# Performance work log

Hardware: AMD Instinct MI355X
Metric: run time of the kernel (lower is better)

## Reference

```python
import jax, jax.numpy as jnp
import numpy as np

N_EMBD = 768
N_HEAD = 12
HEAD_DIM = N_EMBD // N_HEAD


def setup_inputs() -> dict:
    key = jax.random.key(0)
    ks = jax.random.split(key, 5)
    B, S = 4, 2048
    x = jax.random.normal(ks[0], (B, S, N_EMBD), dtype=jnp.float32)
    scale = 0.02
    w_attn = jax.random.normal(ks[1], (N_EMBD, 3 * N_EMBD), dtype=jnp.float32) * scale
    b_attn = jnp.zeros((3 * N_EMBD,), dtype=jnp.float32)
    w_proj = jax.random.normal(ks[2], (N_EMBD, N_EMBD), dtype=jnp.float32) * scale
    b_proj = jnp.zeros((N_EMBD,), dtype=jnp.float32)
    return {"x": x, "w_attn": w_attn, "b_attn": b_attn, "w_proj": w_proj, "b_proj": b_proj}


def reference(x, w_attn, b_attn, w_proj, b_proj):
    B, S, E = x.shape
    qkv = x @ w_attn + b_attn  # [B,S,3E]
    q, k, v = jnp.split(qkv, 3, axis=2)
    # [B,H,S,D]
    q = q.reshape(B, S, N_HEAD, HEAD_DIM).transpose(0, 2, 1, 3)
    k = k.reshape(B, S, N_HEAD, HEAD_DIM).transpose(0, 2, 1, 3)
    v = v.reshape(B, S, N_HEAD, HEAD_DIM).transpose(0, 2, 1, 3)
    scores = jnp.einsum('bhqd,bhkd->bhqk', q, k) / jnp.sqrt(jnp.float32(HEAD_DIM))
    causal = jnp.tril(jnp.ones((S, S), dtype=bool))
    scores = jnp.where(causal[None, None], scores, jnp.float32(-jnp.inf))
    weights = jax.nn.softmax(scores, axis=-1)
    out = jnp.einsum('bhqk,bhkd->bhqd', weights, v)
    out = out.transpose(0, 2, 1, 3).reshape(B, S, E)
    return out @ w_proj + b_proj
```

## Files before the change

### kernel.cpp

```cpp
#include <hip/hip_runtime.h>
#include <hip/hip_bf16.h>

typedef __attribute__((ext_vector_type(8))) __bf16 bf16x8;
typedef __attribute__((ext_vector_type(4))) __bf16 bf16x4;
typedef __attribute__((ext_vector_type(4))) float f32x4;

#define E_ 768
#define HEADS 12
#define HD 64
#define S_ 2048
#define B_ 4

__device__ inline unsigned short f2bf(float f) {
    union { float f; unsigned int u; } x{f};
    unsigned int r = x.u + 0x7FFFu + ((x.u >> 16) & 1u);
    return (unsigned short)(r >> 16);
}

__device__ inline float fexp2(float x) { return __builtin_amdgcn_exp2f(x); }

__global__ void cvt_kernel(const float* __restrict__ in, unsigned short* __restrict__ out, int n4) {
    int i = blockIdx.x * blockDim.x + threadIdx.x;
    if (i < n4) {
        float4 v = reinterpret_cast<const float4*>(in)[i];
        ushort4 o;
        o.x = f2bf(v.x); o.y = f2bf(v.y); o.z = f2bf(v.z); o.w = f2bf(v.w);
        reinterpret_cast<ushort4*>(out)[i] = o;
    }
}

__global__ void transpose_cvt(const float* __restrict__ w, unsigned short* __restrict__ wT,
                              int K, int N) {
    __shared__ float tile[32][33];
    int n0 = blockIdx.x * 32, k0 = blockIdx.y * 32;
    int tx = threadIdx.x, ty = threadIdx.y;
    tile[ty][tx] = w[(size_t)(k0 + ty) * N + n0 + tx];
    __syncthreads();
    wT[(size_t)(n0 + ty) * K + k0 + tx] = f2bf(tile[tx][ty]);
}

template<int MODE>
__global__ __launch_bounds__(256) void gemm16(
    const unsigned short* __restrict__ A, const unsigned short* __restrict__ Bt,
    const float* __restrict__ bias,
    unsigned short* __restrict__ Qo, unsigned short* __restrict__ Ko,
    unsigned short* __restrict__ Vt, float* __restrict__ Of,
    int M, int N, int K)
{
    constexpr int BN = (MODE == 0) ? 128 : 64;
    constexpr int NJ = BN / 32;
    __shared__ unsigned short Sh[128 * 128];
    unsigned short* Ash = Sh;
    unsigned short* Bsh = Sh + 128 * 64;

    const int nbx = N / BN;
    const int nwg = (M >> 7) * nbx;
    const int cpx = nwg >> 3;
    const int orig = blockIdx.x;
    const int wgid = (orig & 7) * cpx + (orig >> 3);
    const int row0 = (wgid / nbx) * 128;
    const int col0 = (wgid % nbx) * BN;

    const int t = threadIdx.x;
    const int w = t >> 6, lane = t & 63;
    const int lr = lane & 15, lc = lane >> 4;
    const int wrow = (w >> 1) * 64;
    const int wcol = (w & 1) * (BN / 2);

    const int srow = lane >> 3;
    const int sslot = lane & 7;

    f32x4 acc[4][NJ] = {};

    for (int k0 = 0; k0 < K; k0 += 64) {
#pragma unroll
        for (int j = 0; j < 4; j++) {
            const int rbase = j * 32 + w * 8;
            const unsigned short* ga = A + (size_t)(row0 + rbase + srow) * K + k0 + sslot * 8;
            __builtin_amdgcn_global_load_lds(
                (const __attribute__((address_space(1))) void*)ga,
                (__attribute__((address_space(3))) void*)&Ash[rbase * 64], 16, 0, 0);
        }
#pragma unroll
        for (int j = 0; j < NJ; j++) {
            const int rbase = j * 32 + w * 8;
            const unsigned short* gb = Bt + (size_t)(col0 + rbase + srow) * K + k0 + sslot * 8;
            __builtin_amdgcn_global_load_lds(
                (const __attribute__((address_space(1))) void*)gb,
                (__attribute__((address_space(3))) void*)&Bsh[rbase * 64], 16, 0, 0);
        }
        __syncthreads();

#pragma unroll
        for (int ks = 0; ks < 2; ks++) {
            bf16x8 a[4], b[NJ];
#pragma unroll
            for (int i = 0; i < 4; i++)
                a[i] = *reinterpret_cast<const bf16x8*>(&Ash[(wrow + i * 16 + lr) * 64 + ks * 32 + lc * 8]);
#pragma unroll
            for (int j2 = 0; j2 < NJ; j2++)
                b[j2] = *reinterpret_cast<const bf16x8*>(&Bsh[(wcol + j2 * 16 + lr) * 64 + ks * 32 + lc * 8]);
#pragma unroll
            for (int i = 0; i < 4; i++)
#pragma unroll
                for (int j2 = 0; j2 < NJ; j2++)
                    acc[i][j2] = __builtin_amdgcn_mfma_f32_16x16x32_bf16(a[i], b[j2], acc[i][j2], 0, 0, 0);
        }
        __syncthreads();
    }

    if constexpr (MODE == 0) {
        const int bb = row0 >> 11;
        const int s0 = row0 & (S_ - 1);
        if (col0 >= 2 * E_) {
#pragma unroll
            for (int i = 0; i < 4; i++)
#pragma unroll
                for (int j = 0; j < 4; j++) {
                    const int c = wcol + j * 16 + lr;
                    const float bv = bias[col0 + c];
#pragma unroll
                    for (int r = 0; r < 4; r++) {
                        const int row = wrow + i * 16 + lc * 4 + r;
                        Sh[c * 128 + (row ^ ((c & 15) << 3))] = f2bf(acc[i][j][r] + bv);
                    }
                }
            __syncthreads();
            const int nnb = col0 - 2 * E_;
#pragma unroll
            for (int pass = 0; pass < 8; pass++) {
                const int c = pass * 16 + (t >> 4);
                const int sL = (t & 15) * 8;
                bf16x8 vv = *reinterpret_cast<const bf16x8*>(&Sh[c * 128 + (sL ^ ((c & 15) << 3))]);
                const int h = (nnb + c) >> 6, d = c & 63;
                const size_t bh = (size_t)(bb * HEADS + h);
                *reinterpret_cast<bf16x8*>(&Vt[(bh * HD + d) * S_ + s0 + sL]) = vv;
            }
            return;
        }
        const int which = col0 / E_;
        const float qsc = (which == 0) ? 0.18033688f : 1.0f;
        unsigned short* dst = (which == 0) ? Qo : Ko;
        const int hbase = (col0 - which * E_) >> 6;
#pragma unroll
        for (int i = 0; i < 4; i++)
#pragma unroll
            for (int j = 0; j < 4; j++) {
                const int c = wcol + j * 16 + lr;
                const float bv = bias[col0 + c];
#pragma unroll
                for (int r = 0; r < 4; r++) {
                    const int row = wrow + i * 16 + lc * 4 + r;
                    Sh[row * 128 + (c ^ ((row & 15) << 3))] = f2bf((acc[i][j][r] + bv) * qsc);
                }
            }
        __syncthreads();
#pragma unroll
        for (int pass = 0; pass < 8; pass++) {
            const int row = pass * 16 + (t >> 4);
            const int c2 = (t & 15) * 8;
            bf16x8 vv = *reinterpret_cast<const bf16x8*>(&Sh[row * 128 + (c2 ^ ((row & 15) << 3))]);
            const int h = hbase + (c2 >> 6), d = c2 & 63;
            const size_t bh = (size_t)(bb * HEADS + h);
            *reinterpret_cast<bf16x8*>(&dst[(bh * S_ + s0 + row) * HD + d]) = vv;
        }
    } else {
#pragma unroll
        for (int i = 0; i < 4; i++)
#pragma unroll
            for (int j = 0; j < NJ; j++) {
                int col = col0 + wcol + j * 16 + lr;
                float bv = bias[col];
#pragma unroll
                for (int r = 0; r < 4; r++) {
                    int row = row0 + wrow + i * 16 + lc * 4 + r;
                    Of[(size_t)row * N + col] = acc[i][j][r] + bv;
                }
            }
    }
}

__global__ __launch_bounds__(256) void attn_kernel(
    const unsigned short* __restrict__ Q, const unsigned short* __restrict__ Kd,
    const unsigned short* __restrict__ Vt, unsigned short* __restrict__ O)
{
    __shared__ unsigned short Ksh[128 * 64];
    __shared__ unsigned short Vsh[64 * 128];

    const int t = threadIdx.x;
    const int w = t >> 6, lane = t & 63;
    const int lr = lane & 15, lc = lane >> 4;
    const int g = blockIdx.x;
    const int bp = g / 48;
    const int bh = g - bp * 48;
    const int tTL = bp, tTH = 31 - bp;
    const int qLrow0 = tTL * 64 + w * 16;
    const int qHrow0 = tTH * 64 + w * 16;
    const int nL = (tTL + 2) >> 1;

    const unsigned short* Qb = Q + (size_t)bh * S_ * HD;
    const unsigned short* Kb = Kd + (size_t)bh * S_ * HD;
    const unsigned short* Vb = Vt + (size_t)bh * HD * S_;

    const int srK = t >> 3, ssK = t & 7;
    const int kws = ((ssK ^ (srK & 7)) << 3);
    const int srV = t >> 4, ssV = t & 15;
    const int vs1 = (ssV >> 2) * 4 + (ssV & 1) * 2;
    const int voff = ((ssV >> 1) & 1) * 4;
    const int vws1 = ((vs1 ^ srV) << 3) + voff;
    const int vws2 = (((vs1 + 1) ^ srV) << 3) + voff;
    const int r7 = lr & 7;

    const unsigned short* KbS = Kb + (size_t)srK * HD + ssK * 8;
    const unsigned short* VbS = Vb + (size_t)srV * S_ + ssV * 8;

    bf16x8 aqL[2], aqH[2];
#pragma unroll
    for (int dc = 0; dc < 2; dc++) {
        aqL[dc] = *reinterpret_cast<const bf16x8*>(Qb + (size_t)(qLrow0 + lr) * HD + dc * 32 + lc * 8);
        aqH[dc] = *reinterpret_cast<const bf16x8*>(Qb + (size_t)(qHrow0 + lr) * HD + dc * 32 + lc * 8);
    }

    f32x4 o[4] = {};
    float m = -INFINITY, l = 0.f;

    int bb = bh / HEADS, hh = bh - bb * HEADS;

    bf16x8 kreg[4], vreg[4];
#pragma unroll
    for (int i = 0; i < 4; i++) {
        kreg[i] = *reinterpret_cast<const bf16x8*>(KbS + i * 32 * HD);
        vreg[i] = *reinterpret_cast<const bf16x8*>(VbS + i * 16 * S_);
    }

    bf16x8 aq0 = aqL[0], aq1 = aqL[1];
    int qrow = qLrow0 + lr;

    for (int it = 0; it < 17; ++it) {
        __syncthreads();
#pragma unroll
        for (int i = 0; i < 4; i++) {
            *reinterpret_cast<bf16x8*>(&Ksh[(srK + i * 32) * 64 + kws]) = kreg[i];
            union { bf16x8 v; bf16x4 h[2]; } u;
            u.v = vreg[i];
            const int vrow = (srV + i * 16) * 128;
            *reinterpret_cast<bf16x4*>(&Vsh[vrow + vws1]) = u.h[0];
            *reinterpret_cast<bf16x4*>(&Vsh[vrow + vws2]) = u.h[1];
        }
        __syncthreads();

        if (it + 1 < 17) {
            const int nkv0 = (it + 1 < nL) ? (it + 1) * 128 : (it + 1 - nL) * 128;
#pragma unroll
            for (int i = 0; i < 4; i++) {
                kreg[i] = *reinterpret_cast<const bf16x8*>(KbS + (size_t)nkv0 * HD + i * 32 * HD);
                vreg[i] = *reinterpret_cast<const bf16x8*>(VbS + nkv0 + i * 16 * S_);
            }
        }

        if (it == nL) {
            float lq[4];
#pragma unroll
            for (int r = 0; r < 4; r++) lq[r] = __shfl(l, lc * 4 + r);
#pragma unroll
            for (int r = 0; r < 4; r++) {
                float inv = 1.f / lq[r];
                int qr = qLrow0 + lc * 4 + r;
#pragma unroll
                for (int dt = 0; dt < 4; dt++)
                    O[((size_t)(bb * S_ + qr)) * E_ + hh * HD + dt * 16 + lr] = f2bf(o[dt][r] * inv);
            }
            m = -INFINITY; l = 0.f;
#pragma unroll
            for (int dt = 0; dt < 4; dt++)
#pragma unroll
                for (int r = 0; r < 4; r++) o[dt][r] = 0.f;
            aq0 = aqH[0]; aq1 = aqH[1];
            qrow = qHrow0 + lr;
        }

        const int kv0 = (it < nL) ? it * 128 : (it - nL) * 128;
        const bool needMask = (it == nL - 1) || (it == 16);

        float p[8][4];
#pragma unroll
        for (int kt = 0; kt < 8; kt++) {
            const int row = kt * 16 + lr;
            const bf16x8 bk0 = *reinterpret_cast<const bf16x8*>(&Ksh[row * 64 + ((lc ^ r7) << 3)]);
            const bf16x8 bk1 = *reinterpret_cast<const bf16x8*>(&Ksh[row * 64 + (((4 + lc) ^ r7) << 3)]);
            f32x4 s = {};
            s = __builtin_amdgcn_mfma_f32_16x16x32_bf16(bk0, aq0, s, 0, 0, 0);
            s = __builtin_amdgcn_mfma_f32_16x16x32_bf16(bk1, aq1, s, 0, 0, 0);
#pragma unroll
            for (int r = 0; r < 4; r++) p[kt][r] = s[r];
        }
        if (needMask) {
#pragma unroll
            for (int kt = 0; kt < 8; kt++) {
                const int kbase = kv0 + kt * 16 + lc * 4;
#pragma unroll
                for (int r = 0; r < 4; r++)
                    if (kbase + r > qrow) p[kt][r] = -1e30f;
            }
        }

        float rm = -1e30f;
#pragma unroll
        for (int kt = 0; kt < 8; kt++)
#pragma unroll
            for (int r = 0; r < 4; r++) rm = fmaxf(rm, p[kt][r]);
        rm = fmaxf(rm, __shfl_xor(rm, 16));
        rm = fmaxf(rm, __shfl_xor(rm, 32));

        const bool grow = !__all(rm <= m);
        float mn = m, sc;
        if (grow) {
            mn = fmaxf(m, rm);
            sc = fexp2(m - mn);
        }

        float rs = 0.f;
#pragma unroll
        for (int kt = 0; kt < 8; kt++)
#pragma unroll
            for (int r = 0; r < 4; r++) {
                float e = fexp2(p[kt][r] - mn);
                p[kt][r] = e; rs += e;
            }
        rs += __shfl_xor(rs, 16);
        rs += __shfl_xor(rs, 32);

        if (grow) {
            l = l * sc + rs;
            m = mn;
            float scq[4];
#pragma unroll
            for (int r = 0; r < 4; r++) scq[r] = __shfl(sc, lc * 4 + r);
#pragma unroll
            for (int dt = 0; dt < 4; dt++)
#pragma unroll
                for (int r = 0; r < 4; r++) o[dt][r] *= scq[r];
        } else {
            l += rs;
        }

        bf16x8 ap[4];
#pragma unroll
        for (int kc = 0; kc < 4; kc++) {
            union { bf16x8 v; __bf16 b[8]; } u;
            u.b[0] = (__bf16)p[2 * kc][0];     u.b[1] = (__bf16)p[2 * kc][1];
            u.b[2] = (__bf16)p[2 * kc][2];     u.b[3] = (__bf16)p[2 * kc][3];
            u.b[4] = (__bf16)p[2 * kc + 1][0]; u.b[5] = (__bf16)p[2 * kc + 1][1];
            u.b[6] = (__bf16)p[2 * kc + 1][2]; u.b[7] = (__bf16)p[2 * kc + 1][3];
            ap[kc] = u.v;
        }

#pragma unroll
        for (int dt = 0; dt < 4; dt++) {
            const int row = dt * 16 + lr;
#pragma unroll
            for (int kc = 0; kc < 4; kc++) {
                const bf16x8 bv = *reinterpret_cast<const bf16x8*>(
                    &Vsh[row * 128 + (((kc * 4 + lc) ^ lr) << 3)]);
                o[dt] = __builtin_amdgcn_mfma_f32_16x16x32_bf16(ap[kc], bv, o[dt], 0, 0, 0);
            }
        }
    }

    {
        float lq[4];
#pragma unroll
        for (int r = 0; r < 4; r++) lq[r] = __shfl(l, lc * 4 + r);
#pragma unroll
        for (int r = 0; r < 4; r++) {
            float inv = 1.f / lq[r];
            int qr = qHrow0 + lc * 4 + r;
#pragma unroll
            for (int dt = 0; dt < 4; dt++)
                O[((size_t)(bb * S_ + qr)) * E_ + hh * HD + dt * 16 + lr] = f2bf(o[dt][r] * inv);
        }
    }
}

extern "C" void kernel_launch(void* const* d_in, const int* in_sizes, int n_in,
                              void* d_out, int out_size, void* d_ws, size_t ws_size,
                              hipStream_t stream) {
    const float* x      = (const float*)d_in[0];
    const float* w_attn = (const float*)d_in[1];
    const float* b_attn = (const float*)d_in[2];
    const float* w_proj = (const float*)d_in[3];
    const float* b_proj = (const float*)d_in[4];
    float* out = (float*)d_out;

    char* ws = (char*)d_ws;
    const size_t M = (size_t)B_ * S_;
    unsigned short* xb  = (unsigned short*)(ws);
    unsigned short* waT = (unsigned short*)(ws + 12582912);
    unsigned short* wpT = (unsigned short*)(ws + 16121856);
    unsigned short* Qb  = (unsigned short*)(ws + 17301504);
    unsigned short* Kb  = (unsigned short*)(ws + 29884416);
    unsigned short* Vt  = (unsigned short*)(ws + 42467328);
    unsigned short* AO  = (unsigned short*)(ws + 55050240);

    int n4 = (int)(M * E_ / 4);
    cvt_kernel<<<(n4 + 255) / 256, 256, 0, stream>>>(x, xb, n4);
    transpose_cvt<<<dim3(3 * E_ / 32, E_ / 32), dim3(32, 32), 0, stream>>>(w_attn, waT, E_, 3 * E_);
    transpose_cvt<<<dim3(E_ / 32, E_ / 32), dim3(32, 32), 0, stream>>>(w_proj, wpT, E_, E_);

    gemm16<0><<<1152, 256, 0, stream>>>(
        xb, waT, b_attn, Qb, Kb, Vt, nullptr, (int)M, 3 * E_, E_);

    attn_kernel<<<768, 256, 0, stream>>>(Qb, Kb, Vt, AO);

    gemm16<1><<<768, 256, 0, stream>>>(
        AO, wpT, b_proj, nullptr, nullptr, nullptr, out, (int)M, E_, E_);
}
```

Baseline: 159.0 us.

## Software-pipeline attention loop: overlap QK^T of next tile with softmax/PV of previous

Restructures the attention main loop into epochs in which the QK^T MFMAs for tile e run alongside the softmax and PV MFMAs for tile e-1. V shared memory is double-buffered, and K/V global prefetches are staggered so K is loaded two tiles ahead and V one tile ahead. The aim is to hide softmax latency and LDS stores behind matrix work and cut idle time between dependent phases. In exchange it uses more registers (two score arrays) and more LDS, which could lower occupancy.

```diff
diff --git a/kernel.cpp b/kernel.cpp
--- a/kernel.cpp
+++ b/kernel.cpp
@@ -185,7 +185,7 @@
     const unsigned short* __restrict__ Vt, unsigned short* __restrict__ O)
 {
     __shared__ unsigned short Ksh[128 * 64];
-    __shared__ unsigned short Vsh[64 * 128];
+    __shared__ unsigned short Vsh[2][64 * 128];
 
     const int t = threadIdx.x;
     const int w = t >> 6, lane = t & 63;
@@ -193,9 +193,9 @@
     const int g = blockIdx.x;
     const int bp = g / 48;
     const int bh = g - bp * 48;
-    const int tTL = bp, tTH = 31 - bp;
+    const int tTL = bp;
     const int qLrow0 = tTL * 64 + w * 16;
-    const int qHrow0 = tTH * 64 + w * 16;
+    const int qHrow0 = (31 - bp) * 64 + w * 16;
     const int nL = (tTL + 2) >> 1;
 
     const unsigned short* Qb = Q + (size_t)bh * S_ * HD;
@@ -223,148 +223,174 @@
 
     f32x4 o[4] = {};
     float m = -INFINITY, l = 0.f;
-
-    int bb = bh / HEADS, hh = bh - bb * HEADS;
+    const int bb = bh / HEADS, hh = bh - bb * HEADS;
+
+    auto KV0 = [&](int tIdx) { return (tIdx < nL ? tIdx : tIdx - nL) * 128; };
 
     bf16x8 kreg[4], vreg[4];
 #pragma unroll
-    for (int i = 0; i < 4; i++) {
+    for (int i = 0; i < 4; i++)
         kreg[i] = *reinterpret_cast<const bf16x8*>(KbS + i * 32 * HD);
-        vreg[i] = *reinterpret_cast<const bf16x8*>(VbS + i * 16 * S_);
-    }
-
-    bf16x8 aq0 = aqL[0], aq1 = aqL[1];
-    int qrow = qLrow0 + lr;
-
-    for (int it = 0; it < 17; ++it) {
-        __syncthreads();
+#pragma unroll
+    for (int i = 0; i < 4; i++)
+        *reinterpret_cast<bf16x8*>(&Ksh[(srK + i * 32) * 64 + kws]) = kreg[i];
+    {
+        const int k1 = KV0(1), v0 = 0;
 #pragma unroll
         for (int i = 0; i < 4; i++) {
-            *reinterpret_cast<bf16x8*>(&Ksh[(srK + i * 32) * 64 + kws]) = kreg[i];
-            union { bf16x8 v; bf16x4 h[2]; } u;
-            u.v = vreg[i];
-            const int vrow = (srV + i * 16) * 128;
-            *reinterpret_cast<bf16x4*>(&Vsh[vrow + vws1]) = u.h[0];
-            *reinterpret_cast<bf16x4*>(&Vsh[vrow + vws2]) = u.h[1];
-        }
-        __syncthreads();
-
-        if (it + 1 < 17) {
-            const int nkv0 = (it + 1 < nL) ? (it + 1) * 128 : (it + 1 - nL) * 128;
+            kreg[i] = *reinterpret_cast<const bf16x8*>(KbS + (size_t)k1 * HD + i * 32 * HD);
+            vreg[i] = *reinterpret_cast<const bf16x8*>(VbS + v0 + i * 16 * S_);
+        }
+    }
+    __syncthreads();
+
+    float pA[8][4], pB[8][4];
+
+    auto epoch = [&](int e, float (&pcur)[8][4], float (&pprev)[8][4]) {
+        if (e < 17) {
+            const bf16x8 aq0 = (e < nL) ? aqL[0] : aqH[0];
+            const bf16x8 aq1 = (e < nL) ? aqL[1] : aqH[1];
+#pragma unroll
+            for (int kt = 0; kt < 8; kt++) {
+                const int row = kt * 16 + lr;
+                const bf16x8 bk0 = *reinterpret_cast<const bf16x8*>(&Ksh[row * 64 + ((lc ^ r7) << 3)]);
+                const bf16x8 bk1 = *reinterpret_cast<const bf16x8*>(&Ksh[row * 64 + (((4 + lc) ^ r7) << 3)]);
+                f32x4 s = {};
+                s = __builtin_amdgcn_mfma_f32_16x16x32_bf16(bk0, aq0, s, 0, 0, 0);
+                s = __builtin_amdgcn_mfma_f32_16x16x32_bf16(bk1, aq1, s, 0, 0, 0);
+#pragma unroll
+                for (int r = 0; r < 4; r++) pcur[kt][r] = s[r];
+            }
+            __syncthreads();
 #pragma unroll
             for (int i = 0; i < 4; i++) {
-                kreg[i] = *reinterpret_cast<const bf16x8*>(KbS + (size_t)nkv0 * HD + i * 32 * HD);
-                vreg[i] = *reinterpret_cast<const bf16x8*>(VbS + nkv0 + i * 16 * S_);
-            }
-        }
-
-        if (it == nL) {
-            float lq[4];
-#pragma unroll
-            for (int r = 0; r < 4; r++) lq[r] = __shfl(l, lc * 4 + r);
-#pragma unroll
-            for (int r = 0; r < 4; r++) {
-                float inv = 1.f / lq[r];
-                int qr = qLrow0 + lc * 4 + r;
+                if (e <= 15)
+                    *reinterpret_cast<bf16x8*>(&Ksh[(srK + i * 32) * 64 + kws]) = kreg[i];
+                union { bf16x8 v; bf16x4 h[2]; } u;
+                u.v = vreg[i];
+                const int vrow = (srV + i * 16) * 128;
+                *reinterpret_cast<bf16x4*>(&Vsh[e & 1][vrow + vws1]) = u.h[0];
+                *reinterpret_cast<bf16x4*>(&Vsh[e & 1][vrow + vws2]) = u.h[1];
+            }
+            if (e <= 14) {
+                const int kk = KV0(e + 2);
+#pragma unroll
+                for (int i = 0; i < 4; i++)
+                    kreg[i] = *reinterpret_cast<const bf16x8*>(KbS + (size_t)kk * HD + i * 32 * HD);
+            }
+            if (e <= 15) {
+                const int vv = KV0(e + 1);
+#pragma unroll
+                for (int i = 0; i < 4; i++)
+                    vreg[i] = *reinterpret_cast<const bf16x8*>(VbS + vv + i * 16 * S_);
+            }
+        }
+
+        if (e >= 1) {
+            const int tIdx = e - 1;
+            const bool lightT = tIdx < nL;
+            const int qrow_t = (lightT ? qLrow0 : qHrow0) + lr;
+            const int kv0_t = (lightT ? tIdx : tIdx - nL) * 128;
+            if (tIdx == nL - 1 || tIdx == 16) {
+#pragma unroll
+                for (int kt = 0; kt < 8; kt++) {
+                    const int kbase = kv0_t + kt * 16 + lc * 4;
+#pragma unroll
+                    for (int r = 0; r < 4; r++)
+                        if (kbase + r > qrow_t) pprev[kt][r] = -1e30f;
+                }
+            }
+
+            float rm = -1e30f;
+#pragma unroll
+            for (int kt = 0; kt < 8; kt++)
+#pragma unroll
+                for (int r = 0; r < 4; r++) rm = fmaxf(rm, pprev[kt][r]);
+            rm = fmaxf(rm, __shfl_xor(rm, 16));
+            rm = fmaxf(rm, __shfl_xor(rm, 32));
+
+            const bool grow = !__all(rm <= m);
+            float mn = m, sc;
+            if (grow) {
+                mn = fmaxf(m, rm);
+                sc = fexp2(m - mn);
+            }
+
+            float rs = 0.f;
+#pragma unroll
+            for (int kt = 0; kt < 8; kt++)
+#pragma unroll
+                for (int r = 0; r < 4; r++) {
+                    float ee = fexp2(pprev[kt][r] - mn);
+                    pprev[kt][r] = ee; rs += ee;
+                }
+            rs += __shfl_xor(rs, 16);
+            rs += __shfl_xor(rs, 32);
+
+            if (grow) {
+                l = l * sc + rs;
+                m = mn;
+                float scq[4];
+#pragma unroll
+                for (int r = 0; r < 4; r++) scq[r] = __shfl(sc, lc * 4 + r);
 #pragma unroll
                 for (int dt = 0; dt < 4; dt++)
-                    O[((size_t)(bb * S_ + qr)) * E_ + hh * HD + dt * 16 + lr] = f2bf(o[dt][r] * inv);
-            }
-            m = -INFINITY; l = 0.f;
-#pragma unroll
-            for (int dt = 0; dt < 4; dt++)
-#pragma unroll
-                for (int r = 0; r < 4; r++) o[dt][r] = 0.f;
-            aq0 = aqH[0]; aq1 = aqH[1];
-            qrow = qHrow0 + lr;
-        }
-
-        const int kv0 = (it < nL) ? it * 128 : (it - nL) * 128;
-        const bool needMask = (it == nL - 1) || (it == 16);
-
-        float p[8][4];
-#pragma unroll
-        for (int kt = 0; kt < 8; kt++) {
-            const int row = kt * 16 + lr;
-            const bf16x8 bk0 = *reinterpret_cast<const bf16x8*>(&Ksh[row * 64 + ((lc ^ r7) << 3)]);
-            const bf16x8 bk1 = *reinterpret_cast<const bf16x8*>(&Ksh[row * 64 + (((4 + lc) ^ r7) << 3)]);
-            f32x4 s = {};
-            s = __builtin_amdgcn_mfma_f32_16x16x32_bf16(bk0, aq0, s, 0, 0, 0);
-            s = __builtin_amdgcn_mfma_f32_16x16x32_bf16(bk1, aq1, s, 0, 0, 0);
-#pragma unroll
-            for (int r = 0; r < 4; r++) p[kt][r] = s[r];
-        }
-        if (needMask) {
-#pragma unroll
-            for (int kt = 0; kt < 8; kt++) {
-                const int kbase = kv0 + kt * 16 + lc * 4;
-#pragma unroll
-                for (int r = 0; r < 4; r++)
-                    if (kbase + r > qrow) p[kt][r] = -1e30f;
-            }
-        }
-
-        float rm = -1e30f;
-#pragma unroll
-        for (int kt = 0; kt < 8; kt++)
-#pragma unroll
-            for (int r = 0; r < 4; r++) rm = fmaxf(rm, p[kt][r]);
-        rm = fmaxf(rm, __shfl_xor(rm, 16));
-        rm = fmaxf(rm, __shfl_xor(rm, 32));
-
-        const bool grow = !__all(rm <= m);
-        float mn = m, sc;
-        if (grow) {
-            mn = fmaxf(m, rm);
-            sc = fexp2(m - mn);
-        }
-
-        float rs = 0.f;
-#pragma unroll
-        for (int kt = 0; kt < 8; kt++)
-#pragma unroll
-            for (int r = 0; r < 4; r++) {
-                float e = fexp2(p[kt][r] - mn);
-                p[kt][r] = e; rs += e;
-            }
-        rs += __shfl_xor(rs, 16);
-        rs += __shfl_xor(rs, 32);
-
-        if (grow) {
-            l = l * sc + rs;
-            m = mn;
-            float scq[4];
-#pragma unroll
-            for (int r = 0; r < 4; r++) scq[r] = __shfl(sc, lc * 4 + r);
-#pragma unroll
-            for (int dt = 0; dt < 4; dt++)
-#pragma unroll
-                for (int r = 0; r < 4; r++) o[dt][r] *= scq[r];
-        } else {
-            l += rs;
-        }
-
-        bf16x8 ap[4];
-#pragma unroll
-        for (int kc = 0; kc < 4; kc++) {
-            union { bf16x8 v; __bf16 b[8]; } u;
-            u.b[0] = (__bf16)p[2 * kc][0];     u.b[1] = (__bf16)p[2 * kc][1];
-            u.b[2] = (__bf16)p[2 * kc][2];     u.b[3] = (__bf16)p[2 * kc][3];
-            u.b[4] = (__bf16)p[2 * kc + 1][0]; u.b[5] = (__bf16)p[2 * kc + 1][1];
-            u.b[6] = (__bf16)p[2 * kc + 1][2]; u.b[7] = (__bf16)p[2 * kc + 1][3];
-            ap[kc] = u.v;
-        }
-
-#pragma unroll
-        for (int dt = 0; dt < 4; dt++) {
-            const int row = dt * 16 + lr;
+#pragma unroll
+                    for (int r = 0; r < 4; r++) o[dt][r] *= scq[r];
+            } else {
+                l += rs;
+            }
+
+            bf16x8 ap[4];
 #pragma unroll
             for (int kc = 0; kc < 4; kc++) {
-                const bf16x8 bv = *reinterpret_cast<const bf16x8*>(
-                    &Vsh[row * 128 + (((kc * 4 + lc) ^ lr) << 3)]);
-                o[dt] = __builtin_amdgcn_mfma_f32_16x16x32_bf16(ap[kc], bv, o[dt], 0, 0, 0);
-            }
-        }
+                union { bf16x8 v; __bf16 b[8]; } u;
+                u.b[0] = (__bf16)pprev[2 * kc][0];     u.b[1] = (__bf16)pprev[2 * kc][1];
+                u.b[2] = (__bf16)pprev[2 * kc][2];     u.b[3] = (__bf16)pprev[2 * kc][3];
+                u.b[4] = (__bf16)pprev[2 * kc + 1][0]; u.b[5] = (__bf16)pprev[2 * kc + 1][1];
+                u.b[6] = (__bf16)pprev[2 * kc + 1][2]; u.b[7] = (__bf16)pprev[2 * kc + 1][3];
+                ap[kc] = u.v;
+            }
+
+            const unsigned short* Vc = Vsh[tIdx & 1];
+#pragma unroll
+            for (int dt = 0; dt < 4; dt++) {
+                const int row = dt * 16 + lr;
+#pragma unroll
+                for (int kc = 0; kc < 4; kc++) {
+                    const bf16x8 bv = *reinterpret_cast<const bf16x8*>(
+                        &Vc[row * 128 + (((kc * 4 + lc) ^ lr) << 3)]);
+                    o[dt] = __builtin_amdgcn_mfma_f32_16x16x32_bf16(ap[kc], bv, o[dt], 0, 0, 0);
+                }
+            }
+
+            if (tIdx == nL - 1) {
+                float lq[4];
+#pragma unroll
+                for (int r = 0; r < 4; r++) lq[r] = __shfl(l, lc * 4 + r);
+#pragma unroll
+                for (int r = 0; r < 4; r++) {
+                    float inv = 1.f / lq[r];
+                    int qr = qLrow0 + lc * 4 + r;
+#pragma unroll
+                    for (int dt = 0; dt < 4; dt++)
+                        O[((size_t)(bb * S_ + qr)) * E_ + hh * HD + dt * 16 + lr] = f2bf(o[dt][r] * inv);
+                }
+                m = -INFINITY; l = 0.f;
+#pragma unroll
+                for (int dt = 0; dt < 4; dt++)
+#pragma unroll
+                    for (int r = 0; r < 4; r++) o[dt][r] = 0.f;
+            }
+        }
+
+        if (e < 17) __syncthreads();
+    };
+
+#pragma unroll 1
+    for (int ee = 0; ee < 9; ++ee) {
+        epoch(2 * ee, pA, pB);
+        epoch(2 * ee + 1, pB, pA);
     }
 
     {
```

After: 161.5 us. No clear change (+1.6%).

## Split paired causal query tiles into separate blocks, heaviest tiles first

Applied to the files above, without the earlier changes.

Each block used to handle two 64-row query tiles, a light one and a heavy one, giving every block a balanced 17 KV iterations. Now each block handles a single query tile, and the grid doubles to 1536 blocks. Blocks are ordered so the tiles with the most KV iterations launch first. This adds parallelism and removes the mid-loop state reset, but workloads become uneven and K/V staging for the shared range is no longer amortised across two tiles.

```diff
diff --git a/kernel.cpp b/kernel.cpp
--- a/kernel.cpp
+++ b/kernel.cpp
@@ -191,12 +191,10 @@
     const int w = t >> 6, lane = t & 63;
     const int lr = lane & 15, lc = lane >> 4;
     const int g = blockIdx.x;
-    const int bp = g / 48;
-    const int bh = g - bp * 48;
-    const int tTL = bp, tTH = 31 - bp;
-    const int qLrow0 = tTL * 64 + w * 16;
-    const int qHrow0 = tTH * 64 + w * 16;
-    const int nL = (tTL + 2) >> 1;
+    const int tile = 31 - g / 48;
+    const int bh = g % 48;
+    const int qrow0 = tile * 64 + w * 16;
+    const int nIter = (tile + 2) >> 1;
 
     const unsigned short* Qb = Q + (size_t)bh * S_ * HD;
     const unsigned short* Kb = Kd + (size_t)bh * S_ * HD;
@@ -214,17 +212,14 @@
     const unsigned short* KbS = Kb + (size_t)srK * HD + ssK * 8;
     const unsigned short* VbS = Vb + (size_t)srV * S_ + ssV * 8;
 
-    bf16x8 aqL[2], aqH[2];
-#pragma unroll
-    for (int dc = 0; dc < 2; dc++) {
-        aqL[dc] = *reinterpret_cast<const bf16x8*>(Qb + (size_t)(qLrow0 + lr) * HD + dc * 32 + lc * 8);
-        aqH[dc] = *reinterpret_cast<const bf16x8*>(Qb + (size_t)(qHrow0 + lr) * HD + dc * 32 + lc * 8);
-    }
+    bf16x8 aq0, aq1;
+    aq0 = *reinterpret_cast<const bf16x8*>(Qb + (size_t)(qrow0 + lr) * HD + lc * 8);
+    aq1 = *reinterpret_cast<const bf16x8*>(Qb + (size_t)(qrow0 + lr) * HD + 32 + lc * 8);
 
     f32x4 o[4] = {};
     float m = -INFINITY, l = 0.f;
-
-    int bb = bh / HEADS, hh = bh - bb * HEADS;
+    const int bb = bh / HEADS, hh = bh - bb * HEADS;
+    const int qrow = qrow0 + lr;
 
     bf16x8 kreg[4], vreg[4];
 #pragma unroll
@@ -233,10 +228,7 @@
         vreg[i] = *reinterpret_cast<const bf16x8*>(VbS + i * 16 * S_);
     }
 
-    bf16x8 aq0 = aqL[0], aq1 = aqL[1];
-    int qrow = qLrow0 + lr;
-
-    for (int it = 0; it < 17; ++it) {
+    for (int it = 0; it < nIter; ++it) {
         __syncthreads();
 #pragma unroll
         for (int i = 0; i < 4; i++) {
@@ -249,8 +241,8 @@
         }
         __syncthreads();
 
-        if (it + 1 < 17) {
-            const int nkv0 = (it + 1 < nL) ? (it + 1) * 128 : (it + 1 - nL) * 128;
+        if (it + 1 < nIter) {
+            const int nkv0 = (it + 1) * 128;
 #pragma unroll
             for (int i = 0; i < 4; i++) {
                 kreg[i] = *reinterpret_cast<const bf16x8*>(KbS + (size_t)nkv0 * HD + i * 32 * HD);
@@ -258,29 +250,8 @@
             }
         }
 
-        if (it == nL) {
-            float lq[4];
-#pragma unroll
-            for (int r = 0; r < 4; r++) lq[r] = __shfl(l, lc * 4 + r);
-#pragma unroll
-            for (int r = 0; r < 4; r++) {
-                float inv = 1.f / lq[r];
-                int qr = qLrow0 + lc * 4 + r;
-#pragma unroll
-                for (int dt = 0; dt < 4; dt++)
-                    O[((size_t)(bb * S_ + qr)) * E_ + hh * HD + dt * 16 + lr] = f2bf(o[dt][r] * inv);
-            }
-            m = -INFINITY; l = 0.f;
-#pragma unroll
-            for (int dt = 0; dt < 4; dt++)
-#pragma unroll
-                for (int r = 0; r < 4; r++) o[dt][r] = 0.f;
-            aq0 = aqH[0]; aq1 = aqH[1];
-            qrow = qHrow0 + lr;
-        }
-
-        const int kv0 = (it < nL) ? it * 128 : (it - nL) * 128;
-        const bool needMask = (it == nL - 1) || (it == 16);
+        const int kv0 = it * 128;
+        const bool needMask = (it == nIter - 1);
 
         float p[8][4];
 #pragma unroll
@@ -374,7 +345,7 @@
 #pragma unroll
         for (int r = 0; r < 4; r++) {
             float inv = 1.f / lq[r];
-            int qr = qHrow0 + lc * 4 + r;
+            int qr = qrow0 + lc * 4 + r;
 #pragma unroll
             for (int dt = 0; dt < 4; dt++)
                 O[((size_t)(bb * S_ + qr)) * E_ + hh * HD + dt * 16 + lr] = f2bf(o[dt][r] * inv);
@@ -410,7 +381,7 @@
     gemm16<0><<<1152, 256, 0, stream>>>(
         xb, waT, b_attn, Qb, Kb, Vt, nullptr, (int)M, 3 * E_, E_);
 
-    attn_kernel<<<768, 256, 0, stream>>>(Qb, Kb, Vt, AO);
+    attn_kernel<<<1536, 256, 0, stream>>>(Qb, Kb, Vt, AO);
 
     gemm16<1><<<768, 256, 0, stream>>>(
         AO, wpT, b_proj, nullptr, nullptr, nullptr, out, (int)M, E_, E_);
```

After: 152.0 us. -4.4%, faster.
